# Performance work log

Measured on AMD Instinct MI355X. Metric: run time of the kernel, lower is better.

The kernel has to match this reference:

```python
import jax, jax.numpy as jnp
import numpy as np

N_QUBITS = 2
Q_DEPTH = 2
B = 2_097_152


def _rot(phi, theta, omega):
    """PennyLane Rot gate: RZ(omega) @ RY(theta) @ RZ(phi), shape [2,2] complex."""
    ct = jnp.cos(theta * 0.5)
    st = jnp.sin(theta * 0.5)
    m00 = jnp.exp(-0.5j * (phi + omega)) * ct
    m01 = -jnp.exp(0.5j * (phi - omega)) * st
    m10 = jnp.exp(-0.5j * (phi - omega)) * st
    m11 = jnp.exp(0.5j * (phi + omega)) * ct
    return jnp.stack([jnp.stack([m00, m01]), jnp.stack([m10, m11])])


def _circuit(noise, q_weights):
    # AngleEmbedding (RX rotations) applied to |00>: state = RX(a0)|0> (x) RX(a1)|0>
    angles = noise.astype(jnp.float32) * jnp.pi  # original: rand * pi
    c = jnp.cos(angles * 0.5)                    # [B,2]
    s = jnp.sin(angles * 0.5)
    v0 = jnp.stack([c[:, 0] + 0j, -1j * s[:, 0]], axis=1)  # [B,2] amps of qubit 0
    v1 = jnp.stack([c[:, 1] + 0j, -1j * s[:, 1]], axis=1)  # [B,2] amps of qubit 1
    state = v0[:, :, None] * v1[:, None, :]                # [B,2,2] statevector

    # StronglyEntanglingLayers: per layer Rot on each wire, then CNOT ring (r=1)
    for l in range(Q_DEPTH):
        g0 = _rot(q_weights[l, 0, 0], q_weights[l, 0, 1], q_weights[l, 0, 2])
        g1 = _rot(q_weights[l, 1, 0], q_weights[l, 1, 1], q_weights[l, 1, 2])
        state = jnp.einsum('ij,bjk->bik', g0, state)  # gate on qubit 0
        state = jnp.einsum('ij,bkj->bki', g1, state)  # gate on qubit 1
        # CNOT(control=0, target=1): flip qubit-1 index where qubit-0 == 1
        state = jnp.stack([state[:, 0, :], state[:, 1, ::-1]], axis=1)
        # CNOT(control=1, target=0): flip qubit-0 index where qubit-1 == 1
        state = jnp.stack([state[:, :, 0], state[:, ::-1, 1]], axis=2)

    probs = jnp.abs(state) ** 2  # [B,2,2]
    z0 = probs[:, 0, :].sum(-1) - probs[:, 1, :].sum(-1)  # <Z> on wire 0
    z1 = probs[:, :, 0].sum(-1) - probs[:, :, 1].sum(-1)  # <Z> on wire 1
    return jnp.stack([z0, z1], axis=1).astype(jnp.float32)  # [B,2]


def setup_inputs() -> dict:
    key = jax.random.key(0)
    k1, k2 = jax.random.split(key)
    noise = jax.random.uniform(k1, (B, N_QUBITS), dtype=jnp.float32)
    q_weights = 0.1 * jax.random.normal(k2, (Q_DEPTH, N_QUBITS, 3), dtype=jnp.float32)
    return {"noise": noise, "q_weights": q_weights}


def reference(noise, q_weights):
    return _circuit(noise, q_weights)
```

## Files before the change

kernel.cpp:

```cpp
#include <hip/hip_runtime.h>
#include <math.h>


struct Cx { float re, im; };
__device__ inline Cx cmul(Cx a, Cx b){ return {a.re*b.re - a.im*b.im, a.re*b.im + a.im*b.re}; }
__device__ inline Cx cmadd2(Cx a, Cx x, Cx b, Cx y){
  Cx p = cmul(a,x), q = cmul(b,y);
  return { p.re + q.re, p.im + q.im };
}

__device__ inline float quadform(const float* __restrict__ A,
                                 float r0, float r1, float r2, float r3) {
  float t0 = A[0]*r0  + A[1]*r1  + A[2]*r2  + A[3]*r3;
  float t1 = A[4]*r0  + A[5]*r1  + A[6]*r2  + A[7]*r3;
  float t2 = A[8]*r0  + A[9]*r1  + A[10]*r2 + A[11]*r3;
  float t3 = A[12]*r0 + A[13]*r1 + A[14]*r2 + A[15]*r3;
  return r0*t0 + r1*t1 + r2*t2 + r3*t3;
}

__global__ __launch_bounds__(256) void qc_kernel(const float* __restrict__ noise,
                                                 const float* __restrict__ w,
                                                 float* __restrict__ out,
                                                 int nQuads) {
  __shared__ float sA[32];

  if (threadIdx.x == 0) {
    Cx U[4][4];
    for (int r = 0; r < 4; ++r)
      for (int c = 0; c < 4; ++c)
        U[r][c] = { (r == c) ? 1.f : 0.f, 0.f };

    for (int l = 0; l < 2; ++l) {
      Cx g[2][2][2];
      for (int q = 0; q < 2; ++q) {
        float phi = w[l*6 + q*3 + 0];
        float th  = w[l*6 + q*3 + 1];
        float om  = w[l*6 + q*3 + 2];
        float st, ct; sincosf(0.5f*th, &st, &ct);
        float sp, cp; sincosf(0.5f*(phi+om), &sp, &cp);
        float sm, cm; sincosf(0.5f*(phi-om), &sm, &cm);
        g[q][0][0] = {  cp*ct, -sp*ct };
        g[q][0][1] = { -cm*st, -sm*st };
        g[q][1][0] = {  cm*st, -sm*st };
        g[q][1][1] = {  cp*ct,  sp*ct };
      }
      for (int c = 0; c < 4; ++c)
        for (int k = 0; k < 2; ++k) {
          Cx x0 = U[k][c], x1 = U[2+k][c];
          U[k][c]   = cmadd2(g[0][0][0], x0, g[0][0][1], x1);
          U[2+k][c] = cmadd2(g[0][1][0], x0, g[0][1][1], x1);
        }
      for (int c = 0; c < 4; ++c)
        for (int j = 0; j < 2; ++j) {
          Cx x0 = U[2*j][c], x1 = U[2*j+1][c];
          U[2*j][c]   = cmadd2(g[1][0][0], x0, g[1][0][1], x1);
          U[2*j+1][c] = cmadd2(g[1][1][0], x0, g[1][1][1], x1);
        }
      for (int c = 0; c < 4; ++c) { Cx t = U[2][c]; U[2][c] = U[3][c]; U[3][c] = t; }
      for (int c = 0; c < 4; ++c) { Cx t = U[1][c]; U[1][c] = U[3][c]; U[3][c] = t; }
    }

    for (int r = 0; r < 4; ++r) {
      Cx t;
      t = U[r][1]; U[r][1] = {  t.im, -t.re };
      t = U[r][2]; U[r][2] = {  t.im, -t.re };
      t = U[r][3]; U[r][3] = { -t.re, -t.im };
    }

    const float z0s[4] = { 1.f,  1.f, -1.f, -1.f };
    const float z1s[4] = { 1.f, -1.f,  1.f, -1.f };
    for (int a = 0; a < 4; ++a)
      for (int b = 0; b < 4; ++b) {
        float a0 = 0.f, a1 = 0.f;
        for (int r = 0; r < 4; ++r) {
          float d = U[r][a].re*U[r][b].re + U[r][a].im*U[r][b].im;
          a0 += z0s[r]*d;
          a1 += z1s[r]*d;
        }
        sA[a*4 + b]      = a0;
        sA[16 + a*4 + b] = a1;
      }
  }
  __syncthreads();

  float A0[16], A1[16];
  #pragma unroll
  for (int i = 0; i < 16; ++i) { A0[i] = sA[i]; A1[i] = sA[16 + i]; }

  const float4* __restrict__ in4  = (const float4*)noise;
  float4* __restrict__ out4 = (float4*)out;
  const float HPI = 1.57079632679489662f;

  int gid    = blockIdx.x * blockDim.x + threadIdx.x;
  int stride = gridDim.x * blockDim.x;
  for (int i = gid; i < nQuads; i += stride) {
    float4 v = in4[i];
    float4 o;
    {
      float s0, c0, s1, c1;
      __sincosf(v.x * HPI, &s0, &c0);
      __sincosf(v.y * HPI, &s1, &c1);
      float r0 = c0*c1, r1 = c0*s1, r2 = s0*c1, r3 = s0*s1;
      o.x = quadform(A0, r0, r1, r2, r3);
      o.y = quadform(A1, r0, r1, r2, r3);
    }
    {
      float s0, c0, s1, c1;
      __sincosf(v.z * HPI, &s0, &c0);
      __sincosf(v.w * HPI, &s1, &c1);
      float r0 = c0*c1, r1 = c0*s1, r2 = s0*c1, r3 = s0*s1;
      o.z = quadform(A0, r0, r1, r2, r3);
      o.w = quadform(A1, r0, r1, r2, r3);
    }
    out4[i] = o;
  }
}

extern "C" void kernel_launch(void* const* d_in, const int* in_sizes, int n_in,
                              void* d_out, int out_size, void* d_ws, size_t ws_size,
                              hipStream_t stream) {
  const float* noise = (const float*)d_in[0];
  const float* w     = (const float*)d_in[1];
  float* out         = (float*)d_out;

  int nQuads = in_sizes[0] / 4;
  int threads = 256;
  int blocks  = 1024;
  qc_kernel<<<blocks, threads, 0, stream>>>(noise, w, out, nQuads);
}
```

Baseline: 74.82 us.

## Compute circuit matrix per thread and use double-angle trig form

Every thread now builds the 4x4 circuit unitary and quadratic-form matrices in registers, so the single-thread setup, shared memory and __syncthreads are gone. The quadratic form over products of half-angle sines and cosines is rewritten as a 3x3 bilinear form in cos/sin of the full angle, which cuts the per-element FMAs. The main loop also issues four float4 loads up front per thread for more memory-level parallelism. The cost is redundant setup work and extra register pressure in every thread, plus the use of fast __sincosf for the weight angles.

```diff
diff --git a/kernel.cpp b/kernel.cpp
--- a/kernel.cpp
+++ b/kernel.cpp
@@ -9,110 +9,153 @@
   return { p.re + q.re, p.im + q.im };
 }
 
-__device__ inline float quadform(const float* __restrict__ A,
-                                 float r0, float r1, float r2, float r3) {
-  float t0 = A[0]*r0  + A[1]*r1  + A[2]*r2  + A[3]*r3;
-  float t1 = A[4]*r0  + A[5]*r1  + A[6]*r2  + A[7]*r3;
-  float t2 = A[8]*r0  + A[9]*r1  + A[10]*r2 + A[11]*r3;
-  float t3 = A[12]*r0 + A[13]*r1 + A[14]*r2 + A[15]*r3;
-  return r0*t0 + r1*t1 + r2*t2 + r3*t3;
-}
+#define PI_F 3.14159265358979323846f
 
 __global__ __launch_bounds__(256) void qc_kernel(const float* __restrict__ noise,
                                                  const float* __restrict__ w,
                                                  float* __restrict__ out,
                                                  int nQuads) {
-  __shared__ float sA[32];
+  Cx U[4][4];
+  #pragma unroll
+  for (int r = 0; r < 4; ++r)
+    #pragma unroll
+    for (int c = 0; c < 4; ++c)
+      U[r][c] = { (r == c) ? 1.f : 0.f, 0.f };
 
-  if (threadIdx.x == 0) {
-    Cx U[4][4];
-    for (int r = 0; r < 4; ++r)
-      for (int c = 0; c < 4; ++c)
-        U[r][c] = { (r == c) ? 1.f : 0.f, 0.f };
+  #pragma unroll
+  for (int l = 0; l < 2; ++l) {
+    Cx g[2][2][2];
+    #pragma unroll
+    for (int q = 0; q < 2; ++q) {
+      float phi = w[l*6 + q*3 + 0];
+      float th  = w[l*6 + q*3 + 1];
+      float om  = w[l*6 + q*3 + 2];
+      float st, ct; __sincosf(0.5f*th, &st, &ct);
+      float sp, cp; __sincosf(0.5f*(phi+om), &sp, &cp);
+      float sm, cm; __sincosf(0.5f*(phi-om), &sm, &cm);
+      g[q][0][0] = {  cp*ct, -sp*ct };
+      g[q][0][1] = { -cm*st, -sm*st };
+      g[q][1][0] = {  cm*st, -sm*st };
+      g[q][1][1] = {  cp*ct,  sp*ct };
+    }
+    #pragma unroll
+    for (int c = 0; c < 4; ++c)
+      #pragma unroll
+      for (int k = 0; k < 2; ++k) {
+        Cx x0 = U[k][c], x1 = U[2+k][c];
+        U[k][c]   = cmadd2(g[0][0][0], x0, g[0][0][1], x1);
+        U[2+k][c] = cmadd2(g[0][1][0], x0, g[0][1][1], x1);
+      }
+    #pragma unroll
+    for (int c = 0; c < 4; ++c)
+      #pragma unroll
+      for (int j = 0; j < 2; ++j) {
+        Cx x0 = U[2*j][c], x1 = U[2*j+1][c];
+        U[2*j][c]   = cmadd2(g[1][0][0], x0, g[1][0][1], x1);
+        U[2*j+1][c] = cmadd2(g[1][1][0], x0, g[1][1][1], x1);
+      }
+    #pragma unroll
+    for (int c = 0; c < 4; ++c) { Cx t = U[2][c]; U[2][c] = U[3][c]; U[3][c] = t; }
+    #pragma unroll
+    for (int c = 0; c < 4; ++c) { Cx t = U[1][c]; U[1][c] = U[3][c]; U[3][c] = t; }
+  }
 
-    for (int l = 0; l < 2; ++l) {
-      Cx g[2][2][2];
-      for (int q = 0; q < 2; ++q) {
-        float phi = w[l*6 + q*3 + 0];
-        float th  = w[l*6 + q*3 + 1];
-        float om  = w[l*6 + q*3 + 2];
-        float st, ct; sincosf(0.5f*th, &st, &ct);
-        float sp, cp; sincosf(0.5f*(phi+om), &sp, &cp);
-        float sm, cm; sincosf(0.5f*(phi-om), &sm, &cm);
-        g[q][0][0] = {  cp*ct, -sp*ct };
-        g[q][0][1] = { -cm*st, -sm*st };
-        g[q][1][0] = {  cm*st, -sm*st };
-        g[q][1][1] = {  cp*ct,  sp*ct };
-      }
-      for (int c = 0; c < 4; ++c)
-        for (int k = 0; k < 2; ++k) {
-          Cx x0 = U[k][c], x1 = U[2+k][c];
-          U[k][c]   = cmadd2(g[0][0][0], x0, g[0][0][1], x1);
-          U[2+k][c] = cmadd2(g[0][1][0], x0, g[0][1][1], x1);
-        }
-      for (int c = 0; c < 4; ++c)
-        for (int j = 0; j < 2; ++j) {
-          Cx x0 = U[2*j][c], x1 = U[2*j+1][c];
-          U[2*j][c]   = cmadd2(g[1][0][0], x0, g[1][0][1], x1);
-          U[2*j+1][c] = cmadd2(g[1][1][0], x0, g[1][1][1], x1);
-        }
-      for (int c = 0; c < 4; ++c) { Cx t = U[2][c]; U[2][c] = U[3][c]; U[3][c] = t; }
-      for (int c = 0; c < 4; ++c) { Cx t = U[1][c]; U[1][c] = U[3][c]; U[3][c] = t; }
-    }
+  #pragma unroll
+  for (int r = 0; r < 4; ++r) {
+    Cx t;
+    t = U[r][1]; U[r][1] = {  t.im, -t.re };
+    t = U[r][2]; U[r][2] = {  t.im, -t.re };
+    t = U[r][3]; U[r][3] = { -t.re, -t.im };
+  }
 
-    for (int r = 0; r < 4; ++r) {
-      Cx t;
-      t = U[r][1]; U[r][1] = {  t.im, -t.re };
-      t = U[r][2]; U[r][2] = {  t.im, -t.re };
-      t = U[r][3]; U[r][3] = { -t.re, -t.im };
-    }
-
+  float A0f[16], A1f[16];
+  {
     const float z0s[4] = { 1.f,  1.f, -1.f, -1.f };
     const float z1s[4] = { 1.f, -1.f,  1.f, -1.f };
+    #pragma unroll
     for (int a = 0; a < 4; ++a)
+      #pragma unroll
       for (int b = 0; b < 4; ++b) {
         float a0 = 0.f, a1 = 0.f;
+        #pragma unroll
         for (int r = 0; r < 4; ++r) {
           float d = U[r][a].re*U[r][b].re + U[r][a].im*U[r][b].im;
           a0 += z0s[r]*d;
           a1 += z1s[r]*d;
         }
-        sA[a*4 + b]      = a0;
-        sA[16 + a*4 + b] = a1;
+        A0f[a*4+b] = a0;
+        A1f[a*4+b] = a1;
       }
   }
-  __syncthreads();
 
-  float A0[16], A1[16];
-  #pragma unroll
-  for (int i = 0; i < 16; ++i) { A0[i] = sA[i]; A1[i] = sA[16 + i]; }
+  float K0[3][3] = {}, K1[3][3] = {};
+  {
+    const float t00[3] = {0.5f, 0.5f, 0.f};
+    const float t01[3] = {0.f,  0.f,  0.5f};
+    const float t11[3] = {0.5f,-0.5f, 0.f};
+    const float* tv[2][2] = { { t00, t01 }, { t01, t11 } };
+    #pragma unroll
+    for (int i = 0; i < 2; ++i)
+      #pragma unroll
+      for (int j = 0; j < 2; ++j)
+        #pragma unroll
+        for (int k = 0; k < 2; ++k)
+          #pragma unroll
+          for (int l = 0; l < 2; ++l) {
+            float a0 = A0f[(2*i+j)*4 + (2*k+l)];
+            float a1 = A1f[(2*i+j)*4 + (2*k+l)];
+            #pragma unroll
+            for (int p = 0; p < 3; ++p) {
+              float tp = tv[i][k][p];
+              if (tp == 0.f) continue;
+              #pragma unroll
+              for (int qq = 0; qq < 3; ++qq) {
+                float tq = tv[j][l][qq];
+                K0[p][qq] += a0 * tp * tq;
+                K1[p][qq] += a1 * tp * tq;
+              }
+            }
+          }
+  }
 
-  const float4* __restrict__ in4  = (const float4*)noise;
+  const float4* __restrict__ in4 = (const float4*)noise;
   float4* __restrict__ out4 = (float4*)out;
-  const float HPI = 1.57079632679489662f;
 
   int gid    = blockIdx.x * blockDim.x + threadIdx.x;
   int stride = gridDim.x * blockDim.x;
-  for (int i = gid; i < nQuads; i += stride) {
-    float4 v = in4[i];
+
+  auto zpair = [&](float x0, float x1, float& z0, float& z1) {
+    float S0, C0, S1, C1;
+    __sincosf(x0 * PI_F, &S0, &C0);
+    __sincosf(x1 * PI_F, &S1, &C1);
+    float m00 = K0[0][0] + K0[0][1]*C1 + K0[0][2]*S1;
+    float m01 = K0[1][0] + K0[1][1]*C1 + K0[1][2]*S1;
+    float m02 = K0[2][0] + K0[2][1]*C1 + K0[2][2]*S1;
+    z0 = m00 + m01*C0 + m02*S0;
+    float m10 = K1[0][0] + K1[0][1]*C1 + K1[0][2]*S1;
+    float m11 = K1[1][0] + K1[1][1]*C1 + K1[1][2]*S1;
+    float m12 = K1[2][0] + K1[2][1]*C1 + K1[2][2]*S1;
+    z1 = m10 + m11*C0 + m12*S0;
+  };
+
+  if (gid + 3*stride < nQuads) {
+    float4 v0 = in4[gid];
+    float4 v1 = in4[gid +   stride];
+    float4 v2 = in4[gid + 2*stride];
+    float4 v3 = in4[gid + 3*stride];
     float4 o;
-    {
-      float s0, c0, s1, c1;
-      __sincosf(v.x * HPI, &s0, &c0);
-      __sincosf(v.y * HPI, &s1, &c1);
-      float r0 = c0*c1, r1 = c0*s1, r2 = s0*c1, r3 = s0*s1;
-      o.x = quadform(A0, r0, r1, r2, r3);
-      o.y = quadform(A1, r0, r1, r2, r3);
+    zpair(v0.x, v0.y, o.x, o.y); zpair(v0.z, v0.w, o.z, o.w); out4[gid]            = o;
+    zpair(v1.x, v1.y, o.x, o.y); zpair(v1.z, v1.w, o.z, o.w); out4[gid +   stride] = o;
+    zpair(v2.x, v2.y, o.x, o.y); zpair(v2.z, v2.w, o.z, o.w); out4[gid + 2*stride] = o;
+    zpair(v3.x, v3.y, o.x, o.y); zpair(v3.z, v3.w, o.z, o.w); out4[gid + 3*stride] = o;
+  } else {
+    for (int i = gid; i < nQuads; i += stride) {
+      float4 v = in4[i];
+      float4 o;
+      zpair(v.x, v.y, o.x, o.y);
+      zpair(v.z, v.w, o.z, o.w);
+      out4[i] = o;
     }
-    {
-      float s0, c0, s1, c1;
-      __sincosf(v.z * HPI, &s0, &c0);
-      __sincosf(v.w * HPI, &s1, &c1);
-      float r0 = c0*c1, r1 = c0*s1, r2 = s0*c1, r3 = s0*s1;
-      o.z = quadform(A0, r0, r1, r2, r3);
-      o.w = quadform(A1, r0, r1, r2, r3);
-    }
-    out4[i] = o;
   }
 }
 
@@ -124,7 +167,5 @@
   float* out         = (float*)d_out;
 
   int nQuads = in_sizes[0] / 4;
-  int threads = 256;
-  int blocks  = 1024;
-  qc_kernel<<<blocks, threads, 0, stream>>>(noise, w, out, nQuads);
+  qc_kernel<<<1024, 256, 0, stream>>>(noise, w, out, nQuads);
 }
```

After: 75.91 us. No clear change (+1.5%).
